# Optimization experiments

Measured on AMD Instinct MI355X. Metric: run time of the kernel, lower is better.

Reference implementation:

```python
import jax, jax.numpy as jnp
import numpy as np

B, C, H, W = 4, 192, 56, 56


def setup_inputs() -> dict:
    key = jax.random.key(0)
    k1, k2, k3 = jax.random.split(key, 3)
    x = jax.random.normal(k1, (B, C, H, W), dtype=jnp.float32)
    conv_w = jax.random.normal(k2, (C, 2 * C), dtype=jnp.float32) * (1.0 / np.sqrt(2 * C))
    conv_b = jax.random.normal(k3, (C,), dtype=jnp.float32) * 0.01
    bn_gamma = jnp.ones((C,), dtype=jnp.float32)
    bn_beta = jnp.zeros((C,), dtype=jnp.float32)
    bn_mean = jnp.zeros((C,), dtype=jnp.float32)
    bn_var = jnp.ones((C,), dtype=jnp.float32)
    return {"x": x, "conv_w": conv_w, "conv_b": conv_b, "bn_gamma": bn_gamma,
            "bn_beta": bn_beta, "bn_mean": bn_mean, "bn_var": bn_var, "K": 4}


def reference(x, conv_w, conv_b, bn_gamma, bn_beta, bn_mean, bn_var, K):
    b, c, h, w = x.shape
    shifts_h = list(range(0, h, K))          # rolls along H
    shifts_w = list(range(K, w, K))          # rolls along W
    n = len(shifts_h) + len(shifts_w)
    scale = n ** (-0.5)
    # (B, n, C, H, W): all circularly shifted copies (static shift set)
    rolled = jnp.stack([jnp.roll(x, i, axis=2) for i in shifts_h] +
                       [jnp.roll(x, j, axis=3) for j in shifts_w], axis=1)
    # scores: tanh(scale * x * x_rolled), summed over channels -> (B, n, 1, H, W)
    scores = jnp.tanh(rolled * x[:, None] * scale).sum(axis=2, keepdims=True)
    weights = jax.nn.softmax(scores, axis=1)
    out = (rolled * weights).sum(axis=1)     # (B, C, H, W)
    cat = jnp.concatenate([x, out], axis=1)  # (B, 2C, H, W)
    # 1x1 conv as GEMM over channels
    y = jnp.einsum('bchw,oc->bohw', cat, conv_w) + conv_b[None, :, None, None]
    # BatchNorm2d in eval mode (running stats)
    eps = 1e-5
    inv = bn_gamma / jnp.sqrt(bn_var + eps)
    y = (y - bn_mean[None, :, None, None]) * inv[None, :, None, None] + bn_beta[None, :, None, None]
    return jax.nn.gelu(y, approximate=False)
```

## Files before the change

kernel.cpp:

```cpp
#include <hip/hip_runtime.h>
#include <hip/hip_bf16.h>
#include <math.h>

#define BB 4
#define CC 192
#define HH 56
#define WW 56
#define HWW 3136

typedef __attribute__((ext_vector_type(8))) short short8;
typedef __attribute__((ext_vector_type(4))) float f32x4;

__device__ __forceinline__ unsigned short f2b(float f) {
    __hip_bfloat16 h = __float2bfloat16(f);
    return __builtin_bit_cast(unsigned short, h);
}
__device__ __forceinline__ float b2f(unsigned short u) {
    unsigned int x = ((unsigned int)u) << 16;
    return __builtin_bit_cast(float, x);
}
__device__ __forceinline__ void fma4(float4& a, float w, const float4& x) {
    a.x += w * x.x; a.y += w * x.y; a.z += w * x.z; a.w += w * x.w;
}

__global__ __launch_bounds__(256) void k_pre(const float* __restrict__ x,
                                             const float* __restrict__ cw,
                                             float* __restrict__ xt,
                                             unsigned short* __restrict__ cwh,
                                             unsigned short* __restrict__ cwl) {
    int tid = threadIdx.x, bid = blockIdx.x;
    if (bid < 2352) {
        __shared__ float tile[32][33];
        int b = bid / 588, rem = bid % 588;
        int by = rem / 98, bx = rem % 98;
        int tx = tid & 31, ty = tid >> 5;
        int p0 = bx * 32, c0 = by * 32;
#pragma unroll
        for (int i = 0; i < 4; i++) {
            int c = c0 + ty + 8 * i;
            tile[ty + 8 * i][tx] = x[(b * CC + c) * HWW + p0 + tx];
        }
        __syncthreads();
#pragma unroll
        for (int i = 0; i < 4; i++) {
            int p = p0 + ty + 8 * i;
            xt[(size_t)(b * HWW + p) * CC + c0 + tx] = tile[tx][ty + 8 * i];
        }
    } else {
        int i = (bid - 2352) * 256 + tid;
        if (i < 384 * 192) {
            int n = i / 192, k = i % 192;
            float v = (n < 192) ? cw[n * 384 + k] : cw[(n - 192) * 384 + 192 + k];
            unsigned short hi = f2b(v);
            cwh[i] = hi;
            cwl[i] = f2b(v - b2f(hi));
        }
    }
}

__global__ __launch_bounds__(256) void k_mid(const float* __restrict__ xt,
                                             const unsigned short* __restrict__ cwh,
                                             const unsigned short* __restrict__ cwl,
                                             float* __restrict__ sp,
                                             float* __restrict__ u,
                                             float* __restrict__ z) {
    __shared__ __align__(16) char smem[36864];
    int tid = threadIdx.x, bid = blockIdx.x;

    if (bid < 1792) {
        float* Xs = (float*)smem;
        const float K2 = 0.38490017945975050f;
        bool isH = bid < 896;
        int lid = isH ? bid : bid - 896;
        int half = lid & 1;
        int rp = (lid >> 1) & 1;
        int cb2 = lid >> 2;
        int b = cb2 / 56, l0 = cb2 % 56;
        int r0 = rp * 2;

        const float* src = xt + (size_t)(b * HWW) * CC + half * 96;
        for (int idx = tid; idx < 28 * 24; idx += 256) {
            int t2 = idx / 24, cq = idx % 24;
            int pi = (r0 + t2 / 14) + 4 * (t2 % 14);
            int pix = isH ? (pi * WW + l0) : (l0 * WW + pi);
            float4 v = *(const float4*)(src + (size_t)pix * CC + cq * 4);
            *(float4*)&Xs[t2 * 100 + cq * 4] = v;
        }
        __syncthreads();

        int perCls = isH ? 105 : 91;
        if (tid < 2 * perCls) {
            int cls = tid / perCls, p = tid % perCls;
            int a, bb;
            if (isH) {
                a = (int)((sqrtf((float)(8 * p + 1)) - 1.0f) * 0.5f);
                bb = p - (a * (a + 1)) / 2;
            } else {
                int ap = (int)((sqrtf((float)(8 * p + 1)) - 1.0f) * 0.5f);
                bb = p - (ap * (ap + 1)) / 2;
                a = ap + 1;
            }
            const float* pA = &Xs[(cls * 14 + a) * 100];
            const float* pB = &Xs[(cls * 14 + bb) * 100];
            float s0 = 0.f, s1 = 0.f, s2 = 0.f, s3 = 0.f;
#pragma unroll
            for (int q = 0; q < 24; q++) {
                float4 av = *(const float4*)(pA + q * 4);
                float4 bv = *(const float4*)(pB + q * 4);
                s0 += __builtin_amdgcn_rcpf(__expf(av.x * bv.x * K2) + 1.0f);
                s1 += __builtin_amdgcn_rcpf(__expf(av.y * bv.y * K2) + 1.0f);
                s2 += __builtin_amdgcn_rcpf(__expf(av.z * bv.z * K2) + 1.0f);
                s3 += __builtin_amdgcn_rcpf(__expf(av.w * bv.w * K2) + 1.0f);
            }
            float s = 96.0f - 2.0f * (s0 + s1 + s2 + s3);
            int r = r0 + cls;
            size_t base = (size_t)(half * BB + b) * HWW;
            if (isH) {
                int i1 = a - bb;
                int h1 = r + 4 * a, h2 = r + 4 * bb;
                sp[(base + h1 * WW + l0) * 32 + i1] = s;
                if (a != bb) sp[(base + h2 * WW + l0) * 32 + (14 - i1)] = s;
            } else {
                int d = a - bb;
                int w1 = r + 4 * a, w2 = r + 4 * bb;
                sp[(base + l0 * WW + w1) * 32 + 14 + (d - 1)] = s;
                sp[(base + l0 * WW + w2) * 32 + 14 + (13 - d)] = s;
            }
        }
        return;
    }

    {
        unsigned short* Ah = (unsigned short*)smem;
        unsigned short* Al = Ah + 64 * 72;
        unsigned short* Bh = Ah + 2 * 64 * 72;
        unsigned short* Bl = Ah + 3 * 64 * 72;
        float* Ds = (float*)smem;
        int vb = bid - 1792;
        int bm = (vb % 196) * 64, bn = (vb / 196) * 64;
        int lane = tid & 63, wv = tid >> 6;

        f32x4 acc[4] = {{0,0,0,0},{0,0,0,0},{0,0,0,0},{0,0,0,0}};

        for (int kc = 0; kc < 3; kc++) {
#pragma unroll
            for (int r2 = 0; r2 < 2; r2++) {
                int idx = tid + r2 * 256;
                int m = idx >> 3, kq = idx & 7;
                const float* s = xt + (size_t)(bm + m) * CC + kc * 64 + kq * 8;
                float4 v0 = *(const float4*)s;
                float4 v1 = *(const float4*)(s + 4);
                float vv[8] = {v0.x, v0.y, v0.z, v0.w, v1.x, v1.y, v1.z, v1.w};
                unsigned short hi[8], lo[8];
#pragma unroll
                for (int e = 0; e < 8; e++) {
                    hi[e] = f2b(vv[e]);
                    lo[e] = f2b(vv[e] - b2f(hi[e]));
                }
                *(short8*)&Ah[m * 72 + kq * 8] = *(short8*)hi;
                *(short8*)&Al[m * 72 + kq * 8] = *(short8*)lo;
                size_t bo = (size_t)(bn + m) * 192 + kc * 64 + kq * 8;
                *(short8*)&Bh[m * 72 + kq * 8] = *(const short8*)(cwh + bo);
                *(short8*)&Bl[m * 72 + kq * 8] = *(const short8*)(cwl + bo);
            }
            __syncthreads();
            int n0 = wv * 16;
            int k8 = lane >> 4;
            int col = lane & 15;
#pragma unroll
            for (int ks = 0; ks < 64; ks += 32) {
                int koff = ks + k8 * 8;
                short8 bfh = *(const short8*)&Bh[(n0 + col) * 72 + koff];
                short8 bfl = *(const short8*)&Bl[(n0 + col) * 72 + koff];
#pragma unroll
                for (int fm = 0; fm < 4; fm++) {
                    short8 afh = *(const short8*)&Ah[(fm * 16 + col) * 72 + koff];
                    short8 afl = *(const short8*)&Al[(fm * 16 + col) * 72 + koff];
                    acc[fm] = __builtin_amdgcn_mfma_f32_16x16x32_bf16(afh, bfh, acc[fm], 0, 0, 0);
                    acc[fm] = __builtin_amdgcn_mfma_f32_16x16x32_bf16(afl, bfh, acc[fm], 0, 0, 0);
                    acc[fm] = __builtin_amdgcn_mfma_f32_16x16x32_bf16(afh, bfl, acc[fm], 0, 0, 0);
                }
            }
            __syncthreads();
        }
        {
            int col = lane & 15, rowq = lane >> 4;
#pragma unroll
            for (int fm = 0; fm < 4; fm++)
#pragma unroll
                for (int rg = 0; rg < 4; rg++)
                    Ds[(fm * 16 + rowq * 4 + rg) * 68 + wv * 16 + col] = acc[fm][rg];
        }
        __syncthreads();
        {
            int c4 = tid & 15, m0 = tid >> 4;
            int cg = bn + c4 * 4;
            float* dst = (cg < 192) ? u : z;
            int cc = (cg < 192) ? cg : cg - 192;
#pragma unroll
            for (int p = 0; p < 4; p++) {
                int m = m0 + p * 16;
                float4 v = *(float4*)&Ds[m * 68 + c4 * 4];
                *(float4*)&dst[(size_t)(bm + m) * CC + cc] = v;
            }
        }
    }
}

__global__ __launch_bounds__(192) void k_accH(const float* __restrict__ u,
                                              const float* __restrict__ z,
                                              const float* __restrict__ sp,
                                              float* __restrict__ yp) {
    __shared__ float Wt[14 * 56];
    int bid = blockIdx.x, tid = threadIdx.x;
    int b = bid / 56, l0 = bid % 56;

    if (tid < 56) {
        int pix = tid * WW + l0;
        const float4* p0 = (const float4*)&sp[((size_t)(0 * BB + b) * HWW + pix) * 32];
        const float4* p1 = (const float4*)&sp[((size_t)(1 * BB + b) * HWW + pix) * 32];
        float sc[28];
#pragma unroll
        for (int j = 0; j < 7; j++) {
            float4 a = p0[j], v = p1[j];
            sc[4 * j + 0] = a.x + v.x; sc[4 * j + 1] = a.y + v.y;
            sc[4 * j + 2] = a.z + v.z; sc[4 * j + 3] = a.w + v.w;
        }
        float mx = -1e30f;
#pragma unroll
        for (int s = 0; s < 27; s++) mx = fmaxf(mx, sc[s]);
        float sum = 0.f;
#pragma unroll
        for (int s = 0; s < 27; s++) { sc[s] = __expf(sc[s] - mx); sum += sc[s]; }
        float inv = __builtin_amdgcn_rcpf(sum);
#pragma unroll
        for (int i = 0; i < 14; i++) Wt[i * 56 + tid] = sc[i] * inv;
    }
    __syncthreads();
    {
        int r = tid & 3, q = tid >> 2;
        float4 in[14];
#pragma unroll
        for (int t = 0; t < 14; t++) {
            int pix = (r + 4 * t) * WW + l0;
            in[t] = *(const float4*)(z + (size_t)(b * HWW + pix) * CC + q * 4);
        }
        float4 acc[14];
#pragma unroll
        for (int a = 0; a < 14; a++) {
            int pix = (r + 4 * a) * WW + l0;
            acc[a] = *(const float4*)(u + (size_t)(b * HWW + pix) * CC + q * 4);
        }
#pragma unroll
        for (int i = 0; i < 14; i++)
#pragma unroll
            for (int a = 0; a < 14; a++)
                fma4(acc[a], Wt[i * 56 + (r + 4 * a)], in[(a - i + 14) % 14]);
#pragma unroll
        for (int a = 0; a < 14; a++) {
            int pix = (r + 4 * a) * WW + l0;
            *(float4*)(yp + (size_t)(b * HWW + pix) * CC + q * 4) = acc[a];
        }
    }
}

__global__ __launch_bounds__(192) void k_accW(const float* __restrict__ yp,
                                              const float* __restrict__ z,
                                              const float* __restrict__ sp,
                                              const float* __restrict__ cb,
                                              const float* __restrict__ gma,
                                              const float* __restrict__ bta,
                                              const float* __restrict__ mea,
                                              const float* __restrict__ var,
                                              float* __restrict__ y) {
    __shared__ float Wt[14 * 56];
    __shared__ float Ys[56 * 196];
    int bid = blockIdx.x, tid = threadIdx.x;
    int b = bid / 56, l0 = bid % 56;

    if (tid < 56) {
        int pix = l0 * WW + tid;
        const float4* p0 = (const float4*)&sp[((size_t)(0 * BB + b) * HWW + pix) * 32];
        const float4* p1 = (const float4*)&sp[((size_t)(1 * BB + b) * HWW + pix) * 32];
        float sc[28];
#pragma unroll
        for (int j = 0; j < 7; j++) {
            float4 a = p0[j], v = p1[j];
            sc[4 * j + 0] = a.x + v.x; sc[4 * j + 1] = a.y + v.y;
            sc[4 * j + 2] = a.z + v.z; sc[4 * j + 3] = a.w + v.w;
        }
        float mx = -1e30f;
#pragma unroll
        for (int s = 0; s < 27; s++) mx = fmaxf(mx, sc[s]);
        float sum = 0.f;
#pragma unroll
        for (int s = 0; s < 27; s++) { sc[s] = __expf(sc[s] - mx); sum += sc[s]; }
        float inv = __builtin_amdgcn_rcpf(sum);
#pragma unroll
        for (int j = 0; j < 13; j++) Wt[j * 56 + tid] = sc[14 + j] * inv;
    }
    __syncthreads();
    {
        int r = tid & 3, q = tid >> 2;
        float4 in[14];
#pragma unroll
        for (int t = 0; t < 14; t++) {
            int pix = l0 * WW + (r + 4 * t);
            in[t] = *(const float4*)(z + (size_t)(b * HWW + pix) * CC + q * 4);
        }
        float4 acc[14];
#pragma unroll
        for (int a = 0; a < 14; a++) {
            int pix = l0 * WW + (r + 4 * a);
            acc[a] = *(const float4*)(yp + (size_t)(b * HWW + pix) * CC + q * 4);
        }
#pragma unroll
        for (int j = 0; j < 13; j++)
#pragma unroll
            for (int a = 0; a < 14; a++)
                fma4(acc[a], Wt[j * 56 + (r + 4 * a)], in[(a - j - 1 + 14) % 14]);

        float4 bias4 = *(const float4*)&cb[q * 4];
        float4 g4 = *(const float4*)&gma[q * 4];
        float4 bt4 = *(const float4*)&bta[q * 4];
        float4 me4 = *(const float4*)&mea[q * 4];
        float4 va4 = *(const float4*)&var[q * 4];
        float inv0 = g4.x * rsqrtf(va4.x + 1e-5f);
        float inv1 = g4.y * rsqrtf(va4.y + 1e-5f);
        float inv2 = g4.z * rsqrtf(va4.z + 1e-5f);
        float inv3 = g4.w * rsqrtf(va4.w + 1e-5f);
#pragma unroll
        for (int a = 0; a < 14; a++) {
            int w = r + 4 * a;
            float4 t = acc[a];
            t.x = (t.x + bias4.x - me4.x) * inv0 + bt4.x;
            t.y = (t.y + bias4.y - me4.y) * inv1 + bt4.y;
            t.z = (t.z + bias4.z - me4.z) * inv2 + bt4.z;
            t.w = (t.w + bias4.w - me4.w) * inv3 + bt4.w;
            t.x = 0.5f * t.x * (1.0f + erff(t.x * 0.70710678118654752f));
            t.y = 0.5f * t.y * (1.0f + erff(t.y * 0.70710678118654752f));
            t.z = 0.5f * t.z * (1.0f + erff(t.z * 0.70710678118654752f));
            t.w = 0.5f * t.w * (1.0f + erff(t.w * 0.70710678118654752f));
            *(float4*)&Ys[w * 196 + q * 4] = t;
        }
    }
    __syncthreads();
    {
        int c = tid;
#pragma unroll
        for (int w4 = 0; w4 < 14; w4++) {
            float4 v;
            v.x = Ys[(w4 * 4 + 0) * 196 + c];
            v.y = Ys[(w4 * 4 + 1) * 196 + c];
            v.z = Ys[(w4 * 4 + 2) * 196 + c];
            v.w = Ys[(w4 * 4 + 3) * 196 + c];
            *(float4*)&y[(size_t)(b * CC + c) * HWW + l0 * WW + w4 * 4] = v;
        }
    }
}

extern "C" void kernel_launch(void* const* d_in, const int* in_sizes, int n_in,
                              void* d_out, int out_size, void* d_ws, size_t ws_size,
                              hipStream_t stream) {
    const float* x   = (const float*)d_in[0];
    const float* cw  = (const float*)d_in[1];
    const float* cb  = (const float*)d_in[2];
    const float* gma = (const float*)d_in[3];
    const float* bta = (const float*)d_in[4];
    const float* mea = (const float*)d_in[5];
    const float* var = (const float*)d_in[6];
    float* out = (float*)d_out;

    float* ws = (float*)d_ws;
    float*          xt  = ws;
    float*          sp  = ws + 2408448;
    float*          u   = ws + 3211264;
    float*          z   = ws + 5619712;
    float*          yp  = ws + 8028160;
    unsigned short* cwh = (unsigned short*)(ws + 10436608);
    unsigned short* cwl = (unsigned short*)(ws + 10473472);

    k_pre<<<2640, 256, 0, stream>>>(x, cw, xt, cwh, cwl);
    k_mid<<<2968, 256, 0, stream>>>(xt, cwh, cwl, sp, u, z);
    k_accH<<<224, 192, 0, stream>>>(u, z, sp, yp);
    k_accW<<<224, 192, 0, stream>>>(yp, z, sp, cb, gma, bta, mea, var, out);
}
```

Before: 127.9 us.

## Restructure pipeline into three kernels, fusing W-shift accumulation into GEMM epilogue

Moves the pairwise score computation into the front kernel so it reads x directly, with the softmax scale folded into the staged values. The GEMM becomes a separate kernel with 112-row tiles (one image row pair) and computes the W-direction weighted accumulation in its epilogue for the z half. The two accumulation kernels merge into one final kernel that adds u and the W partial, applies the H shifts, then BN and GELU. The final store now writes directly without an LDS transpose. This removes one launch and a round trip of the intermediate, at the cost of uncoalesced strided final stores and a heavier GEMM epilogue.

```diff
diff --git a/kernel.cpp b/kernel.cpp
--- a/kernel.cpp
+++ b/kernel.cpp
@@ -23,14 +23,17 @@
     a.x += w * x.x; a.y += w * x.y; a.z += w * x.z; a.w += w * x.w;
 }
 
-__global__ __launch_bounds__(256) void k_pre(const float* __restrict__ x,
-                                             const float* __restrict__ cw,
-                                             float* __restrict__ xt,
-                                             unsigned short* __restrict__ cwh,
-                                             unsigned short* __restrict__ cwl) {
+__global__ __launch_bounds__(256) void k_front(const float* __restrict__ x,
+                                               const float* __restrict__ cw,
+                                               float* __restrict__ xt,
+                                               unsigned short* __restrict__ cwh,
+                                               unsigned short* __restrict__ cwl,
+                                               float* __restrict__ sp) {
+    __shared__ float S[2800];
     int tid = threadIdx.x, bid = blockIdx.x;
+
     if (bid < 2352) {
-        __shared__ float tile[32][33];
+        float (*tile)[33] = (float (*)[33])S;
         int b = bid / 588, rem = bid % 588;
         int by = rem / 98, bx = rem % 98;
         int tx = tid & 31, ty = tid >> 5;
@@ -46,7 +49,9 @@
             int p = p0 + ty + 8 * i;
             xt[(size_t)(b * HWW + p) * CC + c0 + tx] = tile[tx][ty + 8 * i];
         }
-    } else {
+        return;
+    }
+    if (bid < 2640) {
         int i = (bid - 2352) * 256 + tid;
         if (i < 384 * 192) {
             int n = i / 192, k = i % 192;
@@ -55,174 +60,236 @@
             cwh[i] = hi;
             cwl[i] = f2b(v - b2f(hi));
         }
-    }
-}
-
-__global__ __launch_bounds__(256) void k_mid(const float* __restrict__ xt,
-                                             const unsigned short* __restrict__ cwh,
-                                             const unsigned short* __restrict__ cwl,
-                                             float* __restrict__ sp,
-                                             float* __restrict__ u,
-                                             float* __restrict__ z) {
-    __shared__ __align__(16) char smem[36864];
-    int tid = threadIdx.x, bid = blockIdx.x;
-
-    if (bid < 1792) {
-        float* Xs = (float*)smem;
-        const float K2 = 0.38490017945975050f;
-        bool isH = bid < 896;
-        int lid = isH ? bid : bid - 896;
-        int half = lid & 1;
-        int rp = (lid >> 1) & 1;
-        int cb2 = lid >> 2;
-        int b = cb2 / 56, l0 = cb2 % 56;
-        int r0 = rp * 2;
-
-        const float* src = xt + (size_t)(b * HWW) * CC + half * 96;
-        for (int idx = tid; idx < 28 * 24; idx += 256) {
-            int t2 = idx / 24, cq = idx % 24;
+        return;
+    }
+    int vb = bid - 2640;
+    bool isH = vb < 896;
+    int lid = isH ? vb : vb - 896;
+    int half = lid & 1;
+    int rp = (lid >> 1) & 1;
+    int cb2 = lid >> 2;
+    int b = cb2 / 56, l0 = cb2 % 56;
+    int r0 = rp * 2;
+    const float SC = 0.62040705607059197f;
+
+    if (isH) {
+        for (int idx = tid; idx < 28 * 96; idx += 256) {
+            int t2 = idx / 96, c = idx % 96;
             int pi = (r0 + t2 / 14) + 4 * (t2 % 14);
-            int pix = isH ? (pi * WW + l0) : (l0 * WW + pi);
-            float4 v = *(const float4*)(src + (size_t)pix * CC + cq * 4);
-            *(float4*)&Xs[t2 * 100 + cq * 4] = v;
+            float v = x[(size_t)(b * CC + half * 96 + c) * HWW + pi * WW + l0];
+            S[t2 * 100 + c] = v * SC;
+        }
+    } else {
+        for (int idx = tid; idx < 96 * 14; idx += 256) {
+            int c = idx / 14, k = idx % 14;
+            float2 v = *(const float2*)&x[(size_t)(b * CC + half * 96 + c) * HWW +
+                                          l0 * WW + r0 + 4 * k];
+            S[k * 100 + c]        = v.x * SC;
+            S[(14 + k) * 100 + c] = v.y * SC;
+        }
+    }
+    __syncthreads();
+
+    int perCls = isH ? 105 : 91;
+    if (tid < 2 * perCls) {
+        int cls = tid / perCls, p = tid % perCls;
+        int a, bb;
+        if (isH) {
+            a = (int)((sqrtf((float)(8 * p + 1)) - 1.0f) * 0.5f);
+            bb = p - (a * (a + 1)) / 2;
+        } else {
+            int ap = (int)((sqrtf((float)(8 * p + 1)) - 1.0f) * 0.5f);
+            bb = p - (ap * (ap + 1)) / 2;
+            a = ap + 1;
+        }
+        const float* pA = &S[(cls * 14 + a) * 100];
+        const float* pB = &S[(cls * 14 + bb) * 100];
+        float s0 = 0.f, s1 = 0.f, s2 = 0.f, s3 = 0.f;
+#pragma unroll
+        for (int q = 0; q < 24; q++) {
+            float4 av = *(const float4*)(pA + q * 4);
+            float4 bv = *(const float4*)(pB + q * 4);
+            s0 += __builtin_amdgcn_rcpf(__expf(av.x * bv.x) + 1.0f);
+            s1 += __builtin_amdgcn_rcpf(__expf(av.y * bv.y) + 1.0f);
+            s2 += __builtin_amdgcn_rcpf(__expf(av.z * bv.z) + 1.0f);
+            s3 += __builtin_amdgcn_rcpf(__expf(av.w * bv.w) + 1.0f);
+        }
+        float s = 96.0f - 2.0f * (s0 + s1 + s2 + s3);
+        int r = r0 + cls;
+        size_t base = (size_t)(half * BB + b) * HWW;
+        if (isH) {
+            int i1 = a - bb;
+            int h1 = r + 4 * a, h2 = r + 4 * bb;
+            sp[(base + h1 * WW + l0) * 32 + i1] = s;
+            if (a != bb) sp[(base + h2 * WW + l0) * 32 + (14 - i1)] = s;
+        } else {
+            int d = a - bb;
+            int w1 = r + 4 * a, w2 = r + 4 * bb;
+            sp[(base + l0 * WW + w1) * 32 + 14 + (d - 1)] = s;
+            sp[(base + l0 * WW + w2) * 32 + 14 + (13 - d)] = s;
+        }
+    }
+}
+
+__global__ __launch_bounds__(256) void k_gemm(const float* __restrict__ xt,
+                                              const unsigned short* __restrict__ cwh,
+                                              const unsigned short* __restrict__ cwl,
+                                              const float* __restrict__ sp,
+                                              float* __restrict__ u,
+                                              float* __restrict__ z,
+                                              float* __restrict__ yW) {
+    __shared__ __align__(16) char smem[50688];
+    unsigned short* Ah = (unsigned short*)smem;
+    unsigned short* Al = Ah + 112 * 72;
+    unsigned short* Bh = Ah + 2 * 112 * 72;
+    unsigned short* Bl = Bh + 64 * 72;
+    float* Ds  = (float*)smem;
+    float* WtL = (float*)(smem + 30464);
+
+    int tid = threadIdx.x, lane = tid & 63, wv = tid >> 6;
+    int bm = (blockIdx.x % 112) * 112;
+    int bn = (blockIdx.x / 112) * 64;
+    bool is_z = bn >= 192;
+
+    f32x4 acc[7] = {{0,0,0,0},{0,0,0,0},{0,0,0,0},{0,0,0,0},
+                    {0,0,0,0},{0,0,0,0},{0,0,0,0}};
+
+    for (int kc = 0; kc < 192; kc += 64) {
+        for (int idx = tid; idx < 112 * 8; idx += 256) {
+            int m = idx >> 3, kq = idx & 7;
+            const float* s = xt + (size_t)(bm + m) * CC + kc + kq * 8;
+            float4 v0 = *(const float4*)s;
+            float4 v1 = *(const float4*)(s + 4);
+            float vv[8] = {v0.x, v0.y, v0.z, v0.w, v1.x, v1.y, v1.z, v1.w};
+            unsigned short hi[8], lo[8];
+#pragma unroll
+            for (int e = 0; e < 8; e++) {
+                hi[e] = f2b(vv[e]);
+                lo[e] = f2b(vv[e] - b2f(hi[e]));
+            }
+            *(short8*)&Ah[m * 72 + kq * 8] = *(short8*)hi;
+            *(short8*)&Al[m * 72 + kq * 8] = *(short8*)lo;
+        }
+        {
+            int idx = tid;
+            int n = idx >> 3, kq = idx & 7;
+            size_t bo = (size_t)(bn + n) * 192 + kc + kq * 8;
+            *(short8*)&Bh[n * 72 + kq * 8] = *(const short8*)(cwh + bo);
+            *(short8*)&Bl[n * 72 + kq * 8] = *(const short8*)(cwl + bo);
+            idx = tid + 256; n = idx >> 3; kq = idx & 7;
+            bo = (size_t)(bn + n) * 192 + kc + kq * 8;
+            *(short8*)&Bh[n * 72 + kq * 8] = *(const short8*)(cwh + bo);
+            *(short8*)&Bl[n * 72 + kq * 8] = *(const short8*)(cwl + bo);
         }
         __syncthreads();
-
-        int perCls = isH ? 105 : 91;
-        if (tid < 2 * perCls) {
-            int cls = tid / perCls, p = tid % perCls;
-            int a, bb;
-            if (isH) {
-                a = (int)((sqrtf((float)(8 * p + 1)) - 1.0f) * 0.5f);
-                bb = p - (a * (a + 1)) / 2;
-            } else {
-                int ap = (int)((sqrtf((float)(8 * p + 1)) - 1.0f) * 0.5f);
-                bb = p - (ap * (ap + 1)) / 2;
-                a = ap + 1;
+        int k8 = lane >> 4;
+        int col = lane & 15;
+#pragma unroll
+        for (int ks = 0; ks < 64; ks += 32) {
+            int koff = ks + k8 * 8;
+            short8 bfh = *(const short8*)&Bh[(wv * 16 + col) * 72 + koff];
+            short8 bfl = *(const short8*)&Bl[(wv * 16 + col) * 72 + koff];
+#pragma unroll
+            for (int fm = 0; fm < 7; fm++) {
+                short8 afh = *(const short8*)&Ah[(fm * 16 + col) * 72 + koff];
+                short8 afl = *(const short8*)&Al[(fm * 16 + col) * 72 + koff];
+                acc[fm] = __builtin_amdgcn_mfma_f32_16x16x32_bf16(afh, bfh, acc[fm], 0, 0, 0);
+                acc[fm] = __builtin_amdgcn_mfma_f32_16x16x32_bf16(afl, bfh, acc[fm], 0, 0, 0);
+                acc[fm] = __builtin_amdgcn_mfma_f32_16x16x32_bf16(afh, bfl, acc[fm], 0, 0, 0);
             }
-            const float* pA = &Xs[(cls * 14 + a) * 100];
-            const float* pB = &Xs[(cls * 14 + bb) * 100];
-            float s0 = 0.f, s1 = 0.f, s2 = 0.f, s3 = 0.f;
-#pragma unroll
-            for (int q = 0; q < 24; q++) {
-                float4 av = *(const float4*)(pA + q * 4);
-                float4 bv = *(const float4*)(pB + q * 4);
-                s0 += __builtin_amdgcn_rcpf(__expf(av.x * bv.x * K2) + 1.0f);
-                s1 += __builtin_amdgcn_rcpf(__expf(av.y * bv.y * K2) + 1.0f);
-                s2 += __builtin_amdgcn_rcpf(__expf(av.z * bv.z * K2) + 1.0f);
-                s3 += __builtin_amdgcn_rcpf(__expf(av.w * bv.w * K2) + 1.0f);
-            }
-            float s = 96.0f - 2.0f * (s0 + s1 + s2 + s3);
-            int r = r0 + cls;
-            size_t base = (size_t)(half * BB + b) * HWW;
-            if (isH) {
-                int i1 = a - bb;
-                int h1 = r + 4 * a, h2 = r + 4 * bb;
-                sp[(base + h1 * WW + l0) * 32 + i1] = s;
-                if (a != bb) sp[(base + h2 * WW + l0) * 32 + (14 - i1)] = s;
-            } else {
-                int d = a - bb;
-                int w1 = r + 4 * a, w2 = r + 4 * bb;
-                sp[(base + l0 * WW + w1) * 32 + 14 + (d - 1)] = s;
-                sp[(base + l0 * WW + w2) * 32 + 14 + (13 - d)] = s;
-            }
-        }
-        return;
-    }
+        }
+        __syncthreads();
+    }
+
+    int b = bm / HWW, p0 = bm % HWW;
 
     {
-        unsigned short* Ah = (unsigned short*)smem;
-        unsigned short* Al = Ah + 64 * 72;
-        unsigned short* Bh = Ah + 2 * 64 * 72;
-        unsigned short* Bl = Ah + 3 * 64 * 72;
-        float* Ds = (float*)smem;
-        int vb = bid - 1792;
-        int bm = (vb % 196) * 64, bn = (vb / 196) * 64;
-        int lane = tid & 63, wv = tid >> 6;
-
-        f32x4 acc[4] = {{0,0,0,0},{0,0,0,0},{0,0,0,0},{0,0,0,0}};
-
-        for (int kc = 0; kc < 3; kc++) {
-#pragma unroll
-            for (int r2 = 0; r2 < 2; r2++) {
-                int idx = tid + r2 * 256;
-                int m = idx >> 3, kq = idx & 7;
-                const float* s = xt + (size_t)(bm + m) * CC + kc * 64 + kq * 8;
-                float4 v0 = *(const float4*)s;
-                float4 v1 = *(const float4*)(s + 4);
-                float vv[8] = {v0.x, v0.y, v0.z, v0.w, v1.x, v1.y, v1.z, v1.w};
-                unsigned short hi[8], lo[8];
-#pragma unroll
-                for (int e = 0; e < 8; e++) {
-                    hi[e] = f2b(vv[e]);
-                    lo[e] = f2b(vv[e] - b2f(hi[e]));
-                }
-                *(short8*)&Ah[m * 72 + kq * 8] = *(short8*)hi;
-                *(short8*)&Al[m * 72 + kq * 8] = *(short8*)lo;
-                size_t bo = (size_t)(bn + m) * 192 + kc * 64 + kq * 8;
-                *(short8*)&Bh[m * 72 + kq * 8] = *(const short8*)(cwh + bo);
-                *(short8*)&Bl[m * 72 + kq * 8] = *(const short8*)(cwl + bo);
-            }
-            __syncthreads();
-            int n0 = wv * 16;
-            int k8 = lane >> 4;
-            int col = lane & 15;
-#pragma unroll
-            for (int ks = 0; ks < 64; ks += 32) {
-                int koff = ks + k8 * 8;
-                short8 bfh = *(const short8*)&Bh[(n0 + col) * 72 + koff];
-                short8 bfl = *(const short8*)&Bl[(n0 + col) * 72 + koff];
-#pragma unroll
-                for (int fm = 0; fm < 4; fm++) {
-                    short8 afh = *(const short8*)&Ah[(fm * 16 + col) * 72 + koff];
-                    short8 afl = *(const short8*)&Al[(fm * 16 + col) * 72 + koff];
-                    acc[fm] = __builtin_amdgcn_mfma_f32_16x16x32_bf16(afh, bfh, acc[fm], 0, 0, 0);
-                    acc[fm] = __builtin_amdgcn_mfma_f32_16x16x32_bf16(afl, bfh, acc[fm], 0, 0, 0);
-                    acc[fm] = __builtin_amdgcn_mfma_f32_16x16x32_bf16(afh, bfl, acc[fm], 0, 0, 0);
-                }
-            }
-            __syncthreads();
-        }
-        {
-            int col = lane & 15, rowq = lane >> 4;
-#pragma unroll
-            for (int fm = 0; fm < 4; fm++)
-#pragma unroll
-                for (int rg = 0; rg < 4; rg++)
-                    Ds[(fm * 16 + rowq * 4 + rg) * 68 + wv * 16 + col] = acc[fm][rg];
-        }
-        __syncthreads();
-        {
-            int c4 = tid & 15, m0 = tid >> 4;
-            int cg = bn + c4 * 4;
-            float* dst = (cg < 192) ? u : z;
-            int cc = (cg < 192) ? cg : cg - 192;
-#pragma unroll
-            for (int p = 0; p < 4; p++) {
-                int m = m0 + p * 16;
-                float4 v = *(float4*)&Ds[m * 68 + c4 * 4];
-                *(float4*)&dst[(size_t)(bm + m) * CC + cc] = v;
-            }
-        }
-    }
-}
-
-__global__ __launch_bounds__(192) void k_accH(const float* __restrict__ u,
-                                              const float* __restrict__ z,
-                                              const float* __restrict__ sp,
-                                              float* __restrict__ yp) {
+        int col = lane & 15, rowq = lane >> 4;
+#pragma unroll
+        for (int fm = 0; fm < 7; fm++)
+#pragma unroll
+            for (int rg = 0; rg < 4; rg++)
+                Ds[(fm * 16 + rowq * 4 + rg) * 68 + wv * 16 + col] = acc[fm][rg];
+    }
+    if (is_z && tid < 112) {
+        const float4* q0 = (const float4*)&sp[((size_t)(0 * BB + b) * HWW + p0 + tid) * 32];
+        const float4* q1 = (const float4*)&sp[((size_t)(1 * BB + b) * HWW + p0 + tid) * 32];
+        float sc[28];
+#pragma unroll
+        for (int j = 0; j < 7; j++) {
+            float4 a = q0[j], v = q1[j];
+            sc[4 * j + 0] = a.x + v.x; sc[4 * j + 1] = a.y + v.y;
+            sc[4 * j + 2] = a.z + v.z; sc[4 * j + 3] = a.w + v.w;
+        }
+        float mx = -1e30f;
+#pragma unroll
+        for (int s = 0; s < 27; s++) mx = fmaxf(mx, sc[s]);
+        float sum = 0.f;
+#pragma unroll
+        for (int s = 0; s < 27; s++) { sc[s] = __expf(sc[s] - mx); sum += sc[s]; }
+        float inv = __builtin_amdgcn_rcpf(sum);
+#pragma unroll
+        for (int j = 0; j < 13; j++) WtL[j * 112 + tid] = sc[14 + j] * inv;
+    }
+    __syncthreads();
+
+    {
+        int c4 = tid & 15, m0 = tid >> 4;
+        float* dst = is_z ? z : u;
+        int cc = is_z ? (bn - 192) : bn;
+#pragma unroll
+        for (int p = 0; p < 7; p++) {
+            int m = m0 + p * 16;
+            float4 v = *(float4*)&Ds[m * 68 + c4 * 4];
+            *(float4*)&dst[(size_t)(bm + m) * CC + cc + c4 * 4] = v;
+        }
+    }
+    if (is_z && tid < 128) {
+        int row2 = tid >> 6;
+        int r = (tid >> 4) & 3;
+        int q = tid & 15;
+        int pr = row2 * 56;
+        int cz = bn - 192;
+        float4 in[14];
+#pragma unroll
+        for (int t = 0; t < 14; t++)
+            in[t] = *(const float4*)&Ds[(pr + r + 4 * t) * 68 + q * 4];
+        float4 acw[14] = {};
+#pragma unroll
+        for (int j = 0; j < 13; j++)
+#pragma unroll
+            for (int a = 0; a < 14; a++)
+                fma4(acw[a], WtL[j * 112 + pr + r + 4 * a], in[(a - j - 1 + 14) % 14]);
+#pragma unroll
+        for (int a = 0; a < 14; a++) {
+            int m = pr + r + 4 * a;
+            *(float4*)&yW[(size_t)(bm + m) * CC + cz + q * 4] = acw[a];
+        }
+    }
+}
+
+__global__ __launch_bounds__(192) void k_fin(const float* __restrict__ u,
+                                             const float* __restrict__ z,
+                                             const float* __restrict__ yW,
+                                             const float* __restrict__ sp,
+                                             const float* __restrict__ cb,
+                                             const float* __restrict__ gma,
+                                             const float* __restrict__ bta,
+                                             const float* __restrict__ mea,
+                                             const float* __restrict__ var,
+                                             float* __restrict__ y) {
     __shared__ float Wt[14 * 56];
     int bid = blockIdx.x, tid = threadIdx.x;
     int b = bid / 56, l0 = bid % 56;
 
     if (tid < 56) {
         int pix = tid * WW + l0;
-        const float4* p0 = (const float4*)&sp[((size_t)(0 * BB + b) * HWW + pix) * 32];
-        const float4* p1 = (const float4*)&sp[((size_t)(1 * BB + b) * HWW + pix) * 32];
+        const float4* q0 = (const float4*)&sp[((size_t)(0 * BB + b) * HWW + pix) * 32];
+        const float4* q1 = (const float4*)&sp[((size_t)(1 * BB + b) * HWW + pix) * 32];
         float sc[28];
 #pragma unroll
         for (int j = 0; j < 7; j++) {
-            float4 a = p0[j], v = p1[j];
+            float4 a = q0[j], v = q1[j];
             sc[4 * j + 0] = a.x + v.x; sc[4 * j + 1] = a.y + v.y;
             sc[4 * j + 2] = a.z + v.z; sc[4 * j + 3] = a.w + v.w;
         }
@@ -249,76 +316,17 @@
 #pragma unroll
         for (int a = 0; a < 14; a++) {
             int pix = (r + 4 * a) * WW + l0;
-            acc[a] = *(const float4*)(u + (size_t)(b * HWW + pix) * CC + q * 4);
+            size_t off = (size_t)(b * HWW + pix) * CC + q * 4;
+            float4 uu = *(const float4*)(u + off);
+            float4 ww = *(const float4*)(yW + off);
+            acc[a].x = uu.x + ww.x; acc[a].y = uu.y + ww.y;
+            acc[a].z = uu.z + ww.z; acc[a].w = uu.w + ww.w;
         }
 #pragma unroll
         for (int i = 0; i < 14; i++)
 #pragma unroll
             for (int a = 0; a < 14; a++)
                 fma4(acc[a], Wt[i * 56 + (r + 4 * a)], in[(a - i + 14) % 14]);
-#pragma unroll
-        for (int a = 0; a < 14; a++) {
-            int pix = (r + 4 * a) * WW + l0;
-            *(float4*)(yp + (size_t)(b * HWW + pix) * CC + q * 4) = acc[a];
-        }
-    }
-}
-
-__global__ __launch_bounds__(192) void k_accW(const float* __restrict__ yp,
-                                              const float* __restrict__ z,
-                                              const float* __restrict__ sp,
-                                              const float* __restrict__ cb,
-                                              const float* __restrict__ gma,
-                                              const float* __restrict__ bta,
-                                              const float* __restrict__ mea,
-                                              const float* __restrict__ var,
-                                              float* __restrict__ y) {
-    __shared__ float Wt[14 * 56];
-    __shared__ float Ys[56 * 196];
-    int bid = blockIdx.x, tid = threadIdx.x;
-    int b = bid / 56, l0 = bid % 56;
-
-    if (tid < 56) {
-        int pix = l0 * WW + tid;
-        const float4* p0 = (const float4*)&sp[((size_t)(0 * BB + b) * HWW + pix) * 32];
-        const float4* p1 = (const float4*)&sp[((size_t)(1 * BB + b) * HWW + pix) * 32];
-        float sc[28];
-#pragma unroll
-        for (int j = 0; j < 7; j++) {
-            float4 a = p0[j], v = p1[j];
-            sc[4 * j + 0] = a.x + v.x; sc[4 * j + 1] = a.y + v.y;
-            sc[4 * j + 2] = a.z + v.z; sc[4 * j + 3] = a.w + v.w;
-        }
-        float mx = -1e30f;
-#pragma unroll
-        for (int s = 0; s < 27; s++) mx = fmaxf(mx, sc[s]);
-        float sum = 0.f;
-#pragma unroll
-        for (int s = 0; s < 27; s++) { sc[s] = __expf(sc[s] - mx); sum += sc[s]; }
-        float inv = __builtin_amdgcn_rcpf(sum);
-#pragma unroll
-        for (int j = 0; j < 13; j++) Wt[j * 56 + tid] = sc[14 + j] * inv;
-    }
-    __syncthreads();
-    {
-        int r = tid & 3, q = tid >> 2;
-        float4 in[14];
-#pragma unroll
-        for (int t = 0; t < 14; t++) {
-            int pix = l0 * WW + (r + 4 * t);
-            in[t] = *(const float4*)(z + (size_t)(b * HWW + pix) * CC + q * 4);
-        }
-        float4 acc[14];
-#pragma unroll
-        for (int a = 0; a < 14; a++) {
-            int pix = l0 * WW + (r + 4 * a);
-            acc[a] = *(const float4*)(yp + (size_t)(b * HWW + pix) * CC + q * 4);
-        }
-#pragma unroll
-        for (int j = 0; j < 13; j++)
-#pragma unroll
-            for (int a = 0; a < 14; a++)
-                fma4(acc[a], Wt[j * 56 + (r + 4 * a)], in[(a - j - 1 + 14) % 14]);
 
         float4 bias4 = *(const float4*)&cb[q * 4];
         float4 g4 = *(const float4*)&gma[q * 4];
@@ -331,7 +339,7 @@
         float inv3 = g4.w * rsqrtf(va4.w + 1e-5f);
 #pragma unroll
         for (int a = 0; a < 14; a++) {
-            int w = r + 4 * a;
+            int h = r + 4 * a;
             float4 t = acc[a];
             t.x = (t.x + bias4.x - me4.x) * inv0 + bt4.x;
             t.y = (t.y + bias4.y - me4.y) * inv1 + bt4.y;
@@ -341,20 +349,11 @@
             t.y = 0.5f * t.y * (1.0f + erff(t.y * 0.70710678118654752f));
             t.z = 0.5f * t.z * (1.0f + erff(t.z * 0.70710678118654752f));
             t.w = 0.5f * t.w * (1.0f + erff(t.w * 0.70710678118654752f));
-            *(float4*)&Ys[w * 196 + q * 4] = t;
-        }
-    }
-    __syncthreads();
-    {
-        int c = tid;
-#pragma unroll
-        for (int w4 = 0; w4 < 14; w4++) {
-            float4 v;
-            v.x = Ys[(w4 * 4 + 0) * 196 + c];
-            v.y = Ys[(w4 * 4 + 1) * 196 + c];
-            v.z = Ys[(w4 * 4 + 2) * 196 + c];
-            v.w = Ys[(w4 * 4 + 3) * 196 + c];
-            *(float4*)&y[(size_t)(b * CC + c) * HWW + l0 * WW + w4 * 4] = v;
+            size_t yb = (size_t)(b * CC + q * 4) * HWW + h * WW + l0;
+            y[yb] = t.x;
+            y[yb + HWW] = t.y;
+            y[yb + 2 * HWW] = t.z;
+            y[yb + 3 * HWW] = t.w;
         }
     }
 }
@@ -376,12 +375,11 @@
     float*          sp  = ws + 2408448;
     float*          u   = ws + 3211264;
     float*          z   = ws + 5619712;
-    float*          yp  = ws + 8028160;
+    float*          yW  = ws + 8028160;
     unsigned short* cwh = (unsigned short*)(ws + 10436608);
     unsigned short* cwl = (unsigned short*)(ws + 10473472);
 
-    k_pre<<<2640, 256, 0, stream>>>(x, cw, xt, cwh, cwl);
-    k_mid<<<2968, 256, 0, stream>>>(xt, cwh, cwl, sp, u, z);
-    k_accH<<<224, 192, 0, stream>>>(u, z, sp, yp);
-    k_accW<<<224, 192, 0, stream>>>(yp, z, sp, cb, gma, bta, mea, var, out);
-}
+    k_front<<<4432, 256, 0, stream>>>(x, cw, xt, cwh, cwl, sp);
+    k_gemm<<<672, 256, 0, stream>>>(xt, cwh, cwl, sp, u, z, yW);
+    k_fin<<<224, 192, 0, stream>>>(u, z, yW, sp, cb, gma, bta, mea, var, out);
+}
```

After: 147.1 us. +15.0%, slower.

## Fuse H-roll and W-roll accumulation kernels into one row-tiled kernel

Applied to the files above, without the earlier changes.

Merges the separate H-direction and W-direction weighted-roll accumulation kernels into a single kernel per (batch, row). W-rolls use register-resident row data, and H-rolls stream the shifted rows of z directly from global memory. This removes the yp intermediate write and read and one kernel launch. In exchange, H-roll reads go through a serial loop of global loads with less register reuse, so the kernel may become more latency-bound.

```diff
diff --git a/kernel.cpp b/kernel.cpp
--- a/kernel.cpp
+++ b/kernel.cpp
@@ -207,22 +207,28 @@
     }
 }
 
-__global__ __launch_bounds__(192) void k_accH(const float* __restrict__ u,
-                                              const float* __restrict__ z,
-                                              const float* __restrict__ sp,
-                                              float* __restrict__ yp) {
-    __shared__ float Wt[14 * 56];
+__global__ __launch_bounds__(192) void k_fin(const float* __restrict__ u,
+                                             const float* __restrict__ z,
+                                             const float* __restrict__ sp,
+                                             const float* __restrict__ cb,
+                                             const float* __restrict__ gma,
+                                             const float* __restrict__ bta,
+                                             const float* __restrict__ mea,
+                                             const float* __restrict__ var,
+                                             float* __restrict__ y) {
+    __shared__ float Wt[27 * 56];
+    __shared__ float Ys[56 * 196];
     int bid = blockIdx.x, tid = threadIdx.x;
-    int b = bid / 56, l0 = bid % 56;
+    int b = bid / 56, h = bid % 56;
 
     if (tid < 56) {
-        int pix = tid * WW + l0;
-        const float4* p0 = (const float4*)&sp[((size_t)(0 * BB + b) * HWW + pix) * 32];
-        const float4* p1 = (const float4*)&sp[((size_t)(1 * BB + b) * HWW + pix) * 32];
+        int pix = h * WW + tid;
+        const float4* q0 = (const float4*)&sp[((size_t)(0 * BB + b) * HWW + pix) * 32];
+        const float4* q1 = (const float4*)&sp[((size_t)(1 * BB + b) * HWW + pix) * 32];
         float sc[28];
 #pragma unroll
         for (int j = 0; j < 7; j++) {
-            float4 a = p0[j], v = p1[j];
+            float4 a = q0[j], v = q1[j];
             sc[4 * j + 0] = a.x + v.x; sc[4 * j + 1] = a.y + v.y;
             sc[4 * j + 2] = a.z + v.z; sc[4 * j + 3] = a.w + v.w;
         }
@@ -234,92 +240,37 @@
         for (int s = 0; s < 27; s++) { sc[s] = __expf(sc[s] - mx); sum += sc[s]; }
         float inv = __builtin_amdgcn_rcpf(sum);
 #pragma unroll
-        for (int i = 0; i < 14; i++) Wt[i * 56 + tid] = sc[i] * inv;
+        for (int s = 0; s < 27; s++) Wt[s * 56 + tid] = sc[s] * inv;
     }
     __syncthreads();
     {
         int r = tid & 3, q = tid >> 2;
-        float4 in[14];
-#pragma unroll
-        for (int t = 0; t < 14; t++) {
-            int pix = (r + 4 * t) * WW + l0;
-            in[t] = *(const float4*)(z + (size_t)(b * HWW + pix) * CC + q * 4);
-        }
+        float4 inW[14];
+#pragma unroll
+        for (int t = 0; t < 14; t++)
+            inW[t] = *(const float4*)(z + (size_t)(b * HWW + h * WW + (r + 4 * t)) * CC + q * 4);
         float4 acc[14];
 #pragma unroll
-        for (int a = 0; a < 14; a++) {
-            int pix = (r + 4 * a) * WW + l0;
-            acc[a] = *(const float4*)(u + (size_t)(b * HWW + pix) * CC + q * 4);
-        }
-#pragma unroll
-        for (int i = 0; i < 14; i++)
+        for (int a = 0; a < 14; a++)
+            acc[a] = *(const float4*)(u + (size_t)(b * HWW + h * WW + (r + 4 * a)) * CC + q * 4);
+#pragma unroll
+        for (int j = 0; j < 13; j++)
 #pragma unroll
             for (int a = 0; a < 14; a++)
-                fma4(acc[a], Wt[i * 56 + (r + 4 * a)], in[(a - i + 14) % 14]);
-#pragma unroll
-        for (int a = 0; a < 14; a++) {
-            int pix = (r + 4 * a) * WW + l0;
-            *(float4*)(yp + (size_t)(b * HWW + pix) * CC + q * 4) = acc[a];
-        }
-    }
-}
-
-__global__ __launch_bounds__(192) void k_accW(const float* __restrict__ yp,
-                                              const float* __restrict__ z,
-                                              const float* __restrict__ sp,
-                                              const float* __restrict__ cb,
-                                              const float* __restrict__ gma,
-                                              const float* __restrict__ bta,
-                                              const float* __restrict__ mea,
-                                              const float* __restrict__ var,
-                                              float* __restrict__ y) {
-    __shared__ float Wt[14 * 56];
-    __shared__ float Ys[56 * 196];
-    int bid = blockIdx.x, tid = threadIdx.x;
-    int b = bid / 56, l0 = bid % 56;
-
-    if (tid < 56) {
-        int pix = l0 * WW + tid;
-        const float4* p0 = (const float4*)&sp[((size_t)(0 * BB + b) * HWW + pix) * 32];
-        const float4* p1 = (const float4*)&sp[((size_t)(1 * BB + b) * HWW + pix) * 32];
-        float sc[28];
-#pragma unroll
-        for (int j = 0; j < 7; j++) {
-            float4 a = p0[j], v = p1[j];
-            sc[4 * j + 0] = a.x + v.x; sc[4 * j + 1] = a.y + v.y;
-            sc[4 * j + 2] = a.z + v.z; sc[4 * j + 3] = a.w + v.w;
-        }
-        float mx = -1e30f;
-#pragma unroll
-        for (int s = 0; s < 27; s++) mx = fmaxf(mx, sc[s]);
-        float sum = 0.f;
-#pragma unroll
-        for (int s = 0; s < 27; s++) { sc[s] = __expf(sc[s] - mx); sum += sc[s]; }
-        float inv = __builtin_amdgcn_rcpf(sum);
-#pragma unroll
-        for (int j = 0; j < 13; j++) Wt[j * 56 + tid] = sc[14 + j] * inv;
-    }
-    __syncthreads();
-    {
-        int r = tid & 3, q = tid >> 2;
-        float4 in[14];
-#pragma unroll
-        for (int t = 0; t < 14; t++) {
-            int pix = l0 * WW + (r + 4 * t);
-            in[t] = *(const float4*)(z + (size_t)(b * HWW + pix) * CC + q * 4);
-        }
-        float4 acc[14];
-#pragma unroll
-        for (int a = 0; a < 14; a++) {
-            int pix = l0 * WW + (r + 4 * a);
-            acc[a] = *(const float4*)(yp + (size_t)(b * HWW + pix) * CC + q * 4);
-        }
-#pragma unroll
-        for (int j = 0; j < 13; j++)
-#pragma unroll
-            for (int a = 0; a < 14; a++)
-                fma4(acc[a], Wt[j * 56 + (r + 4 * a)], in[(a - j - 1 + 14) % 14]);
-
+                fma4(acc[a], Wt[(14 + j) * 56 + (r + 4 * a)], inW[(a - j - 1 + 14) % 14]);
+#pragma unroll
+        for (int a = 0; a < 14; a++)
+            fma4(acc[a], Wt[0 * 56 + (r + 4 * a)], inW[a]);
+#pragma unroll 1
+        for (int i = 1; i < 14; i++) {
+            int h2 = h - 4 * i; if (h2 < 0) h2 += 56;
+            const float* zr = z + (size_t)(b * HWW + h2 * WW) * CC + q * 4;
+#pragma unroll
+            for (int a = 0; a < 14; a++) {
+                float4 v = *(const float4*)(zr + (size_t)(r + 4 * a) * CC);
+                fma4(acc[a], Wt[i * 56 + (r + 4 * a)], v);
+            }
+        }
         float4 bias4 = *(const float4*)&cb[q * 4];
         float4 g4 = *(const float4*)&gma[q * 4];
         float4 bt4 = *(const float4*)&bta[q * 4];
@@ -354,7 +305,7 @@
             v.y = Ys[(w4 * 4 + 1) * 196 + c];
             v.z = Ys[(w4 * 4 + 2) * 196 + c];
             v.w = Ys[(w4 * 4 + 3) * 196 + c];
-            *(float4*)&y[(size_t)(b * CC + c) * HWW + l0 * WW + w4 * 4] = v;
+            *(float4*)&y[(size_t)(b * CC + c) * HWW + h * WW + w4 * 4] = v;
         }
     }
 }
@@ -376,12 +327,10 @@
     float*          sp  = ws + 2408448;
     float*          u   = ws + 3211264;
     float*          z   = ws + 5619712;
-    float*          yp  = ws + 8028160;
-    unsigned short* cwh = (unsigned short*)(ws + 10436608);
-    unsigned short* cwl = (unsigned short*)(ws + 10473472);
+    unsigned short* cwh = (unsigned short*)(ws + 8028160);
+    unsigned short* cwl = (unsigned short*)(ws + 8065024);
 
     k_pre<<<2640, 256, 0, stream>>>(x, cw, xt, cwh, cwl);
     k_mid<<<2968, 256, 0, stream>>>(xt, cwh, cwl, sp, u, z);
-    k_accH<<<224, 192, 0, stream>>>(u, z, sp, yp);
-    k_accW<<<224, 192, 0, stream>>>(yp, z, sp, cb, gma, bta, mea, var, out);
-}
+    k_fin<<<224, 192, 0, stream>>>(u, z, sp, cb, gma, bta, mea, var, out);
+}
```

Measured after the change: 135.3 us. 5.7% more time.
